# Kernel tuning notes

Measured on AMD Instinct MI355X. Metric: run time of the kernel, lower is better.

## Reference

```python
import jax, jax.numpy as jnp
import numpy as np

N = 50000   # num nodes
E = 800000  # num edges (avg degree 16)
L = 4       # num_blocks
H = 128     # hidden_dim
CD = 3      # coords_dim
VD = 3      # vel_dim
FD = 16     # node feature dim = node_dim - coords_dim - vel_dim
ED = 16     # edge_dim
DIN = 2 * H + ED + 1  # edge MLP input dim = 273


def setup_inputs() -> dict:
    key = jax.random.key(0)
    ks = jax.random.split(key, 32)
    s = 0.05
    inp = {}
    inp['nodes'] = jax.random.normal(ks[0], (N, CD + VD + FD), jnp.float32)
    # avoid self-loops (start==end) so the coord-diff norm is never exactly 0
    start = jax.random.randint(ks[1], (E,), 0, N)
    off = jax.random.randint(ks[2], (E,), 1, N)
    inp['edge_indices'] = jnp.stack([start, (start + off) % N]).astype(jnp.int64)
    inp['edge_features'] = jax.random.normal(ks[3], (E, ED), jnp.float32)
    # node embedding
    inp['emb_w'] = (jax.random.normal(ks[4], (FD, H)) * s).astype(jnp.float32)
    inp['emb_b'] = jnp.zeros((H,), jnp.float32)
    # per-block params, stacked over L blocks
    def w(k, shape):
        return (jax.random.normal(k, shape) * s).astype(jnp.float32)
    inp['ew1'] = w(ks[5], (L, DIN, H)); inp['eb1'] = jnp.zeros((L, H), jnp.float32)
    inp['ew2'] = w(ks[6], (L, H, H));   inp['eb2'] = jnp.zeros((L, H), jnp.float32)
    inp['cw1'] = w(ks[7], (L, H, H));   inp['cb1'] = jnp.zeros((L, H), jnp.float32)
    inp['cw2'] = w(ks[8], (L, H, CD));  inp['cb2'] = jnp.zeros((L, CD), jnp.float32)
    inp['vw1'] = w(ks[9], (L, H, H));   inp['vb1'] = jnp.zeros((L, H), jnp.float32)
    inp['vw2'] = w(ks[10], (L, H, 1));  inp['vb2'] = jnp.zeros((L, 1), jnp.float32)
    inp['nw1'] = w(ks[11], (L, 2 * H, H)); inp['nb1'] = jnp.zeros((L, H), jnp.float32)
    inp['nw2'] = w(ks[12], (L, H, H));  inp['nb2'] = jnp.zeros((L, H), jnp.float32)
    return inp


def _forward(nodes, edge_features, emb_w, emb_b, ew1, eb1, ew2, eb2,
             cw1, cb1, cw2, cb2, vw1, vb1, vw2, vb2, nw1, nb1, nw2, nb2,
             edge_indices):
    silu = jax.nn.silu
    coords = nodes[:, :CD]
    vels = nodes[:, CD:CD + VD]
    h = nodes[:, CD + VD:] @ emb_w + emb_b  # [N, H]
    start, end = edge_indices[0], edge_indices[1]
    n = coords.shape[0]
    # per-node edge counts for the coordinate mean-aggregation
    cnt = jax.ops.segment_sum(jnp.ones((start.shape[0], 1), coords.dtype),
                              start, num_segments=n)
    cnt = jnp.maximum(cnt, 1.0)
    for l in range(L):
        cd = coords[start] - coords[end]                       # [E, CD]
        nrm = jnp.sqrt(jnp.sum(cd * cd, axis=1, keepdims=True))  # [E, 1]
        x = jnp.concatenate([h[start], h[end], nrm, edge_features], axis=1)
        m = silu(silu(x @ ew1[l] + eb1[l]) @ ew2[l] + eb2[l])  # [E, H]
        # coordinate update: mean-aggregated weighted diffs + velocity term
        ct = cd * (silu(m @ cw1[l] + cb1[l]) @ cw2[l] + cb2[l])
        coords = coords + jax.ops.segment_sum(ct, start, num_segments=n) / cnt
        coords = coords + (silu(h @ vw1[l] + vb1[l]) @ vw2[l] + vb2[l]) * vels
        # node update: sum-aggregated messages
        agg = jax.ops.segment_sum(m, start, num_segments=n)    # [N, H]
        h = h + silu(jnp.concatenate([h, agg], axis=1) @ nw1[l] + nb1[l]) @ nw2[l] + nb2[l]
    return coords  # prediction_type == 'coords'


def reference(nodes, edge_indices, edge_features, emb_w, emb_b,
              ew1, eb1, ew2, eb2, cw1, cb1, cw2, cb2,
              vw1, vb1, vw2, vb2, nw1, nb1, nw2, nb2):
    return _forward(nodes, edge_features, emb_w, emb_b, ew1, eb1, ew2, eb2,
                    cw1, cb1, cw2, cb2, vw1, vb1, vw2, vb2,
                    nw1, nb1, nw2, nb2, edge_indices)
```

## Files before the change

### kernel.cpp

```cpp
#include <hip/hip_runtime.h>

constexpr int NN = 50000;
constexpr int EE = 800000;
constexpr int HH = 128;

typedef __attribute__((ext_vector_type(8))) __bf16 bfv8;
typedef __attribute__((ext_vector_type(4))) float f32x4;
typedef unsigned short u16;

__device__ __forceinline__ u16 f2bf(float x){
  unsigned u = __builtin_bit_cast(unsigned, x);
  u = u + 0x7fffu + ((u >> 16) & 1u);
  return (u16)(u >> 16);
}
__device__ __forceinline__ float fsilu(float x){
  return x * __builtin_amdgcn_rcpf(1.f + __expf(-x));
}

__device__ __forceinline__ void stagecpy(u16* __restrict__ dst, const u16* __restrict__ src, int n16){
  const uint4* s = (const uint4*)src;
  uint4* d = (uint4*)dst;
  for (int i = threadIdx.x; i < n16; i += 256) d[i] = s[i];
}

template<int KSTEPS, int CB>
__device__ __forceinline__ void mmW(const u16* Arows, const u16* __restrict__ Bstage,
                                    const float* __restrict__ bias, int NB, f32x4* acc){
  const int lane = threadIdx.x & 63;
  #pragma unroll
  for (int cb = 0; cb < CB; ++cb){
    int col = cb*16 + (lane & 15);
    float b = (col < NB) ? bias[col] : 0.f;
    acc[cb] = (f32x4){b, b, b, b};
  }
  const int arow = lane & 15;
  const char* abase = (const char*)Arows + arow * 256;
  const int kb = (lane >> 4) * 16;
  const int swz = (arow & 7) << 4;
  const bfv8* bq = (const bfv8*)Bstage + lane;
  #pragma unroll
  for (int ks = 0; ks < KSTEPS; ++ks){
    bfv8 a = *(const bfv8*)(abase + ((ks*64 + kb) ^ swz));
    #pragma unroll
    for (int cb = 0; cb < CB; ++cb)
      acc[cb] = __builtin_amdgcn_mfma_f32_16x16x32_bf16(a, bq[(ks*CB + cb) * 64], acc[cb], 0, 0, 0);
  }
}

template<int CB>
__device__ __forceinline__ void silu_store(const f32x4* acc, u16* dst){
  const int lane = threadIdx.x & 63;
  #pragma unroll
  for (int cb = 0; cb < CB; ++cb){
    #pragma unroll
    for (int j = 0; j < 4; ++j){
      int row = ((lane >> 4) << 2) + j;
      int col = cb*16 + (lane & 15);
      *(u16*)((char*)dst + row*256 + ((col*2) ^ ((row & 7) << 4))) = f2bf(fsilu(acc[cb][j]));
    }
  }
}

struct PackDesc { const float* src; u16* dst; int K; int Nc; int CB; int ksteps; int remap; };
struct PackArgs { PackDesc d[32]; };

__global__ __launch_bounds__(256) void pack_kernel(PackArgs pa){
  PackDesc d = pa.d[blockIdx.x];
  int total = d.ksteps * d.CB * 512;
  for (int p = threadIdx.x; p < total; p += 256){
    int j = p & 7, lane = (p >> 3) & 63, cbk = p >> 9;
    int cb = cbk % d.CB, ks = cbk / d.CB;
    int k = ks*32 + ((lane >> 4) * 8) + j;
    int col = cb*16 + (lane & 15);
    int kk = k;
    if (d.remap && k >= 256) kk = (k < 272) ? (k + 1) : ((k == 272) ? 256 : 0x7fffffff);
    float v = (kk < d.K && col < d.Nc) ? d.src[(size_t)kk * d.Nc + col] : 0.f;
    d.dst[p] = f2bf(v);
  }
}

__global__ __launch_bounds__(256) void embed_kernel(const float* __restrict__ nodes,
    const float* __restrict__ emb_w, const float* __restrict__ emb_b,
    float* __restrict__ hf, u16* __restrict__ hbf, float* __restrict__ coords){
  int t = blockIdx.x * 256 + threadIdx.x;
  int g = t >> 2, q = t & 3;
  if (g >= NN) return;
  const float* x = nodes + (size_t)g * 22;
  float acc[32];
  #pragma unroll
  for (int c = 0; c < 32; ++c) acc[c] = emb_b[q*32 + c];
  for (int k = 0; k < 16; ++k){
    float f = x[6 + k];
    const float* wr = emb_w + k*128 + q*32;
    #pragma unroll
    for (int c = 0; c < 32; ++c) acc[c] += f * wr[c];
  }
  size_t off = (size_t)g * HH + q*32;
  #pragma unroll
  for (int c = 0; c < 32; ++c){ hf[off + c] = acc[c]; hbf[off + c] = f2bf(acc[c]); }
  if (q == 0){
    coords[g*3+0] = x[0]; coords[g*3+1] = x[1]; coords[g*3+2] = x[2];
  }
}

__global__ __launch_bounds__(256) void count_kernel(const int* __restrict__ esrc, int* __restrict__ cnt_i){
  int e = blockIdx.x * 256 + threadIdx.x;
  if (e < EE) atomicAdd(&cnt_i[esrc[e]], 1);
}

__global__ __launch_bounds__(256) void scan_kernel(const int* __restrict__ cnt_i,
    int* __restrict__ row_start, int* __restrict__ fill){
  __shared__ int part[256];
  int t = threadIdx.x;
  int lo = t * 196, hi = lo + 196;
  if (lo > NN) lo = NN;
  if (hi > NN) hi = NN;
  int s = 0;
  for (int i = lo; i < hi; ++i) s += cnt_i[i];
  part[t] = s; __syncthreads();
  for (int d = 1; d < 256; d <<= 1){
    int v = (t >= d) ? part[t-d] : 0;
    __syncthreads();
    part[t] += v;
    __syncthreads();
  }
  int run = part[t] - s;
  for (int i = lo; i < hi; ++i){ row_start[i] = run; fill[i] = run; run += cnt_i[i]; }
  if (t == 255) row_start[NN] = run;
}

__global__ __launch_bounds__(256) void scatter_kernel(const int* __restrict__ esrc,
    const int* __restrict__ edst, int* __restrict__ fill,
    int2* __restrict__ sd_sorted, int* __restrict__ eid_sorted){
  int e = blockIdx.x * 256 + threadIdx.x;
  if (e < EE){
    int s = esrc[e];
    int pos = atomicAdd(&fill[s], 1);
    sd_sorted[pos] = make_int2(s, edst[e]);
    eid_sorted[pos] = e;
  }
}

__global__ __launch_bounds__(256) void edge_kernel(
    const float* __restrict__ coords, const u16* __restrict__ hbf, const float* __restrict__ ef,
    const int2* __restrict__ sd_sorted, const int* __restrict__ eid_sorted,
    const u16* __restrict__ ew1p, const u16* __restrict__ ew2p,
    const u16* __restrict__ cw1p, const u16* __restrict__ cw2p,
    const float* __restrict__ eb1, const float* __restrict__ eb2,
    const float* __restrict__ cb1, const float* __restrict__ cb2,
    float* __restrict__ agg, float* __restrict__ acc_ct){
  __shared__ __align__(16) u16 sStage[16384];
  __shared__ __align__(16) u16 sBuf[4][2048];
  __shared__ float4 s_cdn[64];
  __shared__ int s_src[64];
  __shared__ int s_eid[64];

  const int tid = threadIdx.x, wid = tid >> 6, lane = tid & 63;
  const int R = wid * 16;
  const int e0 = blockIdx.x * 64;

  stagecpy(sStage, ew1p, 2048);

  if (lane < 16){
    int row = R + lane;
    int e = e0 + row;
    int2 sd = sd_sorted[e];
    float cx = coords[sd.x*3+0] - coords[sd.y*3+0];
    float cy = coords[sd.x*3+1] - coords[sd.y*3+1];
    float cz = coords[sd.x*3+2] - coords[sd.y*3+2];
    float nrm = sqrtf(cx*cx + cy*cy + cz*cz);
    s_cdn[row] = make_float4(cx, cy, cz, nrm);
    s_src[row] = sd.x; s_eid[row] = eid_sorted[e];
  }

  const int myrow = R + (lane & 15);
  const int g = lane >> 4;
  int2 sd = sd_sorted[e0 + myrow];
  const u16* hsb = hbf + (size_t)sd.x * HH + g*8;
  const u16* hdb = hbf + (size_t)sd.y * HH + g*8;
  u16* sB = sBuf[wid];
  const bfv8* bqs = (const bfv8*)sStage + lane;

  f32x4 acc[8];
  __syncthreads();
  {
    #pragma unroll
    for (int cb = 0; cb < 8; ++cb){
      float b = eb1[cb*16 + (lane & 15)];
      acc[cb] = (f32x4){b, b, b, b};
    }
    #pragma unroll
    for (int ks = 0; ks < 4; ++ks){
      bfv8 a = *(const bfv8*)(hsb + ks*32);
      #pragma unroll
      for (int cb = 0; cb < 8; ++cb)
        acc[cb] = __builtin_amdgcn_mfma_f32_16x16x32_bf16(a, bqs[(ks*8 + cb)*64], acc[cb], 0, 0, 0);
    }
  }
  __syncthreads();
  stagecpy(sStage, ew1p + 4*8*512, 2048);
  __syncthreads();
  {
    #pragma unroll
    for (int ks = 0; ks < 4; ++ks){
      bfv8 a = *(const bfv8*)(hdb + ks*32);
      #pragma unroll
      for (int cb = 0; cb < 8; ++cb)
        acc[cb] = __builtin_amdgcn_mfma_f32_16x16x32_bf16(a, bqs[(ks*8 + cb)*64], acc[cb], 0, 0, 0);
    }
  }
  __syncthreads();
  stagecpy(sStage, ew1p + 8*8*512, 512);
  __syncthreads();
  {
    const int my_eid = s_eid[myrow];
    union { bfv8 v; u16 s[8]; unsigned u[4]; } at;
    at.u[0] = at.u[1] = at.u[2] = at.u[3] = 0u;
    if (g < 2){
      float4 f0 = *(const float4*)(ef + (size_t)my_eid * 16 + g*8);
      float4 f1 = *(const float4*)(ef + (size_t)my_eid * 16 + g*8 + 4);
      at.u[0] = f2bf(f0.x) | ((unsigned)f2bf(f0.y) << 16);
      at.u[1] = f2bf(f0.z) | ((unsigned)f2bf(f0.w) << 16);
      at.u[2] = f2bf(f1.x) | ((unsigned)f2bf(f1.y) << 16);
      at.u[3] = f2bf(f1.z) | ((unsigned)f2bf(f1.w) << 16);
    } else if (g == 2){
      at.s[0] = f2bf(s_cdn[myrow].w);
    }
    #pragma unroll
    for (int cb = 0; cb < 8; ++cb)
      acc[cb] = __builtin_amdgcn_mfma_f32_16x16x32_bf16(at.v, bqs[cb*64], acc[cb], 0, 0, 0);
  }
  silu_store<8>(acc, sB);

  __syncthreads();
  stagecpy(sStage, ew2p, 2048);
  __syncthreads();
  mmW<4, 8>(sB, sStage, eb2, 128, acc);
  {
    const int rb = (lane >> 4) << 2;
    float run[8];
    #pragma unroll
    for (int cb = 0; cb < 8; ++cb) run[cb] = 0.f;
    #pragma unroll
    for (int j = 0; j < 4; ++j){
      int lrow = rb + j, grow = R + lrow;
      int src = s_src[grow];
      bool flush = (j == 3) || (s_src[grow + 1] != src);
      #pragma unroll
      for (int cb = 0; cb < 8; ++cb){
        int col = cb*16 + (lane & 15);
        float m = fsilu(acc[cb][j]);
        run[cb] += m;
        *(u16*)((char*)sB + lrow*256 + ((col*2) ^ ((lrow & 7) << 4))) = f2bf(m);
      }
      if (flush){
        #pragma unroll
        for (int cb = 0; cb < 8; ++cb){
          int col = cb*16 + (lane & 15);
          atomicAdd(&agg[(size_t)src * HH + col], run[cb]);
          run[cb] = 0.f;
        }
      }
    }
  }

  __syncthreads();
  stagecpy(sStage, cw1p, 2048);
  __syncthreads();
  mmW<4, 8>(sB, sStage, cb1, 128, acc);
  silu_store<8>(acc, sB);

  __syncthreads();
  stagecpy(sStage, cw2p, 256);
  __syncthreads();
  f32x4 a4[1];
  mmW<4, 1>(sB, sStage, cb2, 3, a4);
  {
    int col = lane & 15;
    if (col < 3){
      const int rb = (lane >> 4) << 2;
      float run = 0.f;
      #pragma unroll
      for (int j = 0; j < 4; ++j){
        int grow = R + rb + j;
        float4 cdn = s_cdn[grow];
        float cdv = (col == 0) ? cdn.x : ((col == 1) ? cdn.y : cdn.z);
        run += cdv * a4[0][j];
        int src = s_src[grow];
        if (j == 3 || s_src[grow + 1] != src){
          atomicAdd(&acc_ct[(size_t)src * 3 + col], run);
          run = 0.f;
        }
      }
    }
  }
}

__device__ __forceinline__ void mm_lds1(const u16* Arows, const u16* __restrict__ Bp,
                                        const float* __restrict__ bias, int NB, int CBn,
                                        int KS, f32x4* acc){
  const int lane = threadIdx.x & 63;
  for (int cb = 0; cb < CBn; ++cb){
    int col = cb*16 + (lane & 15);
    float b = (col < NB) ? bias[col] : 0.f;
    acc[cb] = (f32x4){b, b, b, b};
  }
  const int arow = lane & 15;
  const char* abase = (const char*)Arows + arow * 256;
  const int kb = (lane >> 4) * 16;
  const int swz = (arow & 7) << 4;
  const bfv8* __restrict__ bq = (const bfv8*)Bp + lane;
  for (int ks = 0; ks < KS; ++ks){
    bfv8 a = *(const bfv8*)(abase + ((ks*64 + kb) ^ swz));
    for (int cb = 0; cb < CBn; ++cb)
      acc[cb] = __builtin_amdgcn_mfma_f32_16x16x32_bf16(a, bq[(ks*CBn + cb) * 64], acc[cb], 0, 0, 0);
  }
}

__global__ __launch_bounds__(256, 4) void node_kernel(
    float* __restrict__ coords, float* __restrict__ hf, u16* __restrict__ hbf,
    const float* __restrict__ agg, const float* __restrict__ acc_ct, const int* __restrict__ row_start,
    const float* __restrict__ nodes,
    const u16* __restrict__ vw1p, const u16* __restrict__ vw2p,
    const u16* __restrict__ nw1p, const u16* __restrict__ nw2p,
    const float* __restrict__ vb1, const float* __restrict__ vb2,
    const float* __restrict__ nb1, const float* __restrict__ nb2){
  __shared__ __align__(16) u16 sV[4][2048];
  __shared__ float s_vt[64];

  const int tid = threadIdx.x, wid = tid >> 6, lane = tid & 63;
  const int R = wid * 16;
  const int g0 = blockIdx.x * 64;

  const int myrow = R + (lane & 15);
  const int gnode = g0 + myrow;
  const int arow = (gnode < NN) ? gnode : (NN - 1);
  const int g = lane >> 4;
  const u16*  hb = hbf + (size_t)arow * HH + g*8;
  const float* ab = agg + (size_t)arow * HH + g*8;

  f32x4 acc[8];
  {
    const bfv8* __restrict__ bq = (const bfv8*)vw1p + lane;
    #pragma unroll
    for (int cb = 0; cb < 8; ++cb){
      float b = vb1[cb*16 + (lane & 15)];
      acc[cb] = (f32x4){b, b, b, b};
    }
    #pragma unroll
    for (int ks = 0; ks < 4; ++ks){
      bfv8 a = *(const bfv8*)(hb + ks*32);
      #pragma unroll
      for (int cb = 0; cb < 8; ++cb)
        acc[cb] = __builtin_amdgcn_mfma_f32_16x16x32_bf16(a, bq[(ks*8 + cb)*64], acc[cb], 0, 0, 0);
    }
  }
  {
    #pragma unroll
    for (int cb = 0; cb < 8; ++cb){
      #pragma unroll
      for (int j = 0; j < 4; ++j){
        int row = ((lane >> 4) << 2) + j;
        int col = cb*16 + (lane & 15);
        *(u16*)((char*)sV[wid] + row*256 + ((col*2) ^ ((row & 7) << 4))) = f2bf(fsilu(acc[cb][j]));
      }
    }
  }
  f32x4 a1[1];
  mm_lds1(sV[wid], vw2p, vb2, 1, 1, 4, a1);
  if ((lane & 15) == 0){
    #pragma unroll
    for (int j = 0; j < 4; ++j) s_vt[R + ((lane >> 4) << 2) + j] = a1[0][j];
  }
  if (lane < 16){
    int row = R + lane, gg = g0 + row;
    if (gg < NN){
      float cn = (float)(row_start[gg + 1] - row_start[gg]);
      if (cn < 1.f) cn = 1.f;
      float vt = s_vt[row];
      #pragma unroll
      for (int c = 0; c < 3; ++c){
        float val = coords[gg*3 + c] + acc_ct[gg*3 + c] / cn + vt * nodes[(size_t)gg*22 + 3 + c];
        coords[gg*3 + c] = val;
      }
    }
  }

  {
    const bfv8* __restrict__ bq = (const bfv8*)nw1p + lane;
    #pragma unroll
    for (int cb = 0; cb < 8; ++cb){
      float b = nb1[cb*16 + (lane & 15)];
      acc[cb] = (f32x4){b, b, b, b};
    }
    #pragma unroll
    for (int ks = 0; ks < 4; ++ks){
      bfv8 a = *(const bfv8*)(hb + ks*32);
      #pragma unroll
      for (int cb = 0; cb < 8; ++cb)
        acc[cb] = __builtin_amdgcn_mfma_f32_16x16x32_bf16(a, bq[(ks*8 + cb)*64], acc[cb], 0, 0, 0);
    }
    #pragma unroll
    for (int ks = 4; ks < 8; ++ks){
      float4 f0 = *(const float4*)(ab + (ks - 4)*32);
      float4 f1 = *(const float4*)(ab + (ks - 4)*32 + 4);
      union { bfv8 v; unsigned u[4]; } aa;
      aa.u[0] = f2bf(f0.x) | ((unsigned)f2bf(f0.y) << 16);
      aa.u[1] = f2bf(f0.z) | ((unsigned)f2bf(f0.w) << 16);
      aa.u[2] = f2bf(f1.x) | ((unsigned)f2bf(f1.y) << 16);
      aa.u[3] = f2bf(f1.z) | ((unsigned)f2bf(f1.w) << 16);
      #pragma unroll
      for (int cb = 0; cb < 8; ++cb)
        acc[cb] = __builtin_amdgcn_mfma_f32_16x16x32_bf16(aa.v, bq[(ks*8 + cb)*64], acc[cb], 0, 0, 0);
    }
  }
  {
    #pragma unroll
    for (int cb = 0; cb < 8; ++cb){
      #pragma unroll
      for (int j = 0; j < 4; ++j){
        int row = ((lane >> 4) << 2) + j;
        int col = cb*16 + (lane & 15);
        *(u16*)((char*)sV[wid] + row*256 + ((col*2) ^ ((row & 7) << 4))) = f2bf(fsilu(acc[cb][j]));
      }
    }
  }
  mm_lds1(sV[wid], nw2p, nb2, 128, 8, 4, acc);
  {
    #pragma unroll
    for (int cb = 0; cb < 8; ++cb){
      int col = cb*16 + (lane & 15);
      #pragma unroll
      for (int j = 0; j < 4; ++j){
        int row = R + ((lane >> 4) << 2) + j, gg = g0 + row;
        if (gg < NN){
          size_t off = (size_t)gg * HH + col;
          float h = acc[cb][j] + hf[off];
          hf[off] = h;
          hbf[off] = f2bf(h);
        }
      }
    }
  }
}

extern "C" void kernel_launch(void* const* d_in, const int* in_sizes, int n_in,
                              void* d_out, int out_size, void* d_ws, size_t ws_size,
                              hipStream_t stream){
  const float* nodes = (const float*)d_in[0];
  const int*   eidx  = (const int*)d_in[1];
  const float* ef    = (const float*)d_in[2];
  const float* emb_w = (const float*)d_in[3];
  const float* emb_b = (const float*)d_in[4];
  const float* ew1 = (const float*)d_in[5];
  const float* eb1 = (const float*)d_in[6];
  const float* ew2 = (const float*)d_in[7];
  const float* eb2 = (const float*)d_in[8];
  const float* cw1 = (const float*)d_in[9];
  const float* cb1 = (const float*)d_in[10];
  const float* cw2 = (const float*)d_in[11];
  const float* cb2 = (const float*)d_in[12];
  const float* vw1 = (const float*)d_in[13];
  const float* vb1 = (const float*)d_in[14];
  const float* vw2 = (const float*)d_in[15];
  const float* vb2 = (const float*)d_in[16];
  const float* nw1 = (const float*)d_in[17];
  const float* nb1 = (const float*)d_in[18];
  const float* nw2 = (const float*)d_in[19];
  const float* nb2 = (const float*)d_in[20];

  constexpr size_t WS_NEEDED = 78u * 1024u * 1024u;
  if (ws_size < WS_NEEDED) return;

  char* ws = (char*)d_ws;
  size_t off = 0;
  auto alloc = [&](size_t bytes){ void* p = ws + off; off += (bytes + 255) & ~(size_t)255; return p; };
  float* coords   = (float*)alloc((size_t)NN * 3 * 4);
  float* hf       = (float*)alloc((size_t)NN * HH * 4);
  u16*   hbf      = (u16*)  alloc((size_t)NN * HH * 2);
  float* agg      = (float*)alloc((size_t)NN * 131 * 4);
  float* acc_ct   = agg + (size_t)NN * HH;
  int*   cnt_i    = (int*)  alloc((size_t)NN * 4);
  int*   row_start= (int*)  alloc((size_t)(NN + 1) * 4);
  int*   fill     = (int*)  alloc((size_t)NN * 4);
  int2*  sd_sorted= (int2*) alloc((size_t)EE * 8);
  int*   eid_sorted=(int*)  alloc((size_t)EE * 4);

  constexpr int O_EW1 = 0;
  constexpr int O_EW2 = O_EW1 + 9*8*512;
  constexpr int O_CW1 = O_EW2 + 4*8*512;
  constexpr int O_CW2 = O_CW1 + 4*8*512;
  constexpr int O_VW1 = O_CW2 + 4*1*512;
  constexpr int O_VW2 = O_VW1 + 4*8*512;
  constexpr int O_NW1 = O_VW2 + 4*1*512;
  constexpr int O_NW2 = O_NW1 + 8*8*512;
  constexpr int LAYER_PACK = O_NW2 + 4*8*512;
  u16* packs = (u16*)alloc((size_t)LAYER_PACK * 4 * 2);

  PackArgs pa;
  for (int l = 0; l < 4; ++l){
    u16* base = packs + (size_t)l * LAYER_PACK;
    int i = l * 8;
    pa.d[i+0] = { ew1 + (size_t)l*273*128, base + O_EW1, 273, 128, 8, 9, 1 };
    pa.d[i+1] = { ew2 + (size_t)l*128*128, base + O_EW2, 128, 128, 8, 4, 0 };
    pa.d[i+2] = { cw1 + (size_t)l*128*128, base + O_CW1, 128, 128, 8, 4, 0 };
    pa.d[i+3] = { cw2 + (size_t)l*128*3,   base + O_CW2, 128,   3, 1, 4, 0 };
    pa.d[i+4] = { vw1 + (size_t)l*128*128, base + O_VW1, 128, 128, 8, 4, 0 };
    pa.d[i+5] = { vw2 + (size_t)l*128*1,   base + O_VW2, 128,   1, 1, 4, 0 };
    pa.d[i+6] = { nw1 + (size_t)l*256*128, base + O_NW1, 256, 128, 8, 8, 0 };
    pa.d[i+7] = { nw2 + (size_t)l*128*128, base + O_NW2, 128, 128, 8, 4, 0 };
  }

  pack_kernel<<<32, 256, 0, stream>>>(pa);
  embed_kernel<<<(NN*4 + 255)/256, 256, 0, stream>>>(nodes, emb_w, emb_b, hf, hbf, coords);
  hipMemsetAsync(cnt_i, 0, (size_t)NN * 4, stream);
  count_kernel<<<(EE + 255)/256, 256, 0, stream>>>(eidx, cnt_i);
  scan_kernel<<<1, 256, 0, stream>>>(cnt_i, row_start, fill);
  scatter_kernel<<<(EE + 255)/256, 256, 0, stream>>>(eidx, eidx + EE, fill, sd_sorted, eid_sorted);

  for (int l = 0; l < 4; ++l){
    hipMemsetAsync(agg, 0, (size_t)NN * 131 * 4, stream);
    u16* base = packs + (size_t)l * LAYER_PACK;
    edge_kernel<<<EE/64, 256, 0, stream>>>(coords, hbf, ef, sd_sorted, eid_sorted,
        base + O_EW1, base + O_EW2, base + O_CW1, base + O_CW2,
        eb1 + l*128, eb2 + l*128, cb1 + l*128, cb2 + l*3, agg, acc_ct);
    node_kernel<<<(NN + 63)/64, 256, 0, stream>>>(coords, hf, hbf, agg, acc_ct, row_start, nodes,
        base + O_VW1, base + O_VW2, base + O_NW1, base + O_NW2,
        vb1 + l*128, vb2 + l, nb1 + l*128, nb2 + l*128);
  }

  hipMemcpyAsync(d_out, coords, (size_t)NN * 3 * 4, hipMemcpyDeviceToDevice, stream);
}
```

Baseline: 2.096 ms.

## Stage all edge weights once in LDS, double block size, drop per-phase barriers

The edge kernel now runs 512 threads over 128 edges per block. It copies the whole first-layer weight matrix and the second-layer matrix into a larger LDS buffer once at kernel start, which removes the repeated stage/barrier cycles between matmul phases. The coordinate MLP weights (cw1, cw2) are read straight from global memory instead of from LDS. The cost is about 104KB of weight staging plus 32KB of buffers in LDS per block, which limits occupancy to one block per CU, and the cw1/cw2 reads now go through global memory or cache.

Result: slower. 2.403 ms (+14.7%).

```diff
diff --git a/kernel.cpp b/kernel.cpp
--- a/kernel.cpp
+++ b/kernel.cpp
@@ -17,14 +17,8 @@
   return x * __builtin_amdgcn_rcpf(1.f + __expf(-x));
 }
 
-__device__ __forceinline__ void stagecpy(u16* __restrict__ dst, const u16* __restrict__ src, int n16){
-  const uint4* s = (const uint4*)src;
-  uint4* d = (uint4*)dst;
-  for (int i = threadIdx.x; i < n16; i += 256) d[i] = s[i];
-}
-
 template<int KSTEPS, int CB>
-__device__ __forceinline__ void mmW(const u16* Arows, const u16* __restrict__ Bstage,
+__device__ __forceinline__ void mmW(const u16* Arows, const u16* Bp,
                                     const float* __restrict__ bias, int NB, f32x4* acc){
   const int lane = threadIdx.x & 63;
   #pragma unroll
@@ -37,7 +31,7 @@
   const char* abase = (const char*)Arows + arow * 256;
   const int kb = (lane >> 4) * 16;
   const int swz = (arow & 7) << 4;
-  const bfv8* bq = (const bfv8*)Bstage + lane;
+  const bfv8* bq = (const bfv8*)Bp + lane;
   #pragma unroll
   for (int ks = 0; ks < KSTEPS; ++ks){
     bfv8 a = *(const bfv8*)(abase + ((ks*64 + kb) ^ swz));
@@ -141,7 +135,7 @@
   }
 }
 
-__global__ __launch_bounds__(256) void edge_kernel(
+__global__ __launch_bounds__(512) void edge_kernel(
     const float* __restrict__ coords, const u16* __restrict__ hbf, const float* __restrict__ ef,
     const int2* __restrict__ sd_sorted, const int* __restrict__ eid_sorted,
     const u16* __restrict__ ew1p, const u16* __restrict__ ew2p,
@@ -149,17 +143,24 @@
     const float* __restrict__ eb1, const float* __restrict__ eb2,
     const float* __restrict__ cb1, const float* __restrict__ cb2,
     float* __restrict__ agg, float* __restrict__ acc_ct){
-  __shared__ __align__(16) u16 sStage[16384];
-  __shared__ __align__(16) u16 sBuf[4][2048];
-  __shared__ float4 s_cdn[64];
-  __shared__ int s_src[64];
-  __shared__ int s_eid[64];
+  __shared__ __align__(16) u16 sStage[53248];
+  __shared__ __align__(16) u16 sBuf[8][2048];
+  __shared__ float4 s_cdn[128];
+  __shared__ int s_src[128];
+  __shared__ int s_eid[128];
 
   const int tid = threadIdx.x, wid = tid >> 6, lane = tid & 63;
   const int R = wid * 16;
-  const int e0 = blockIdx.x * 64;
-
-  stagecpy(sStage, ew1p, 2048);
+  const int e0 = blockIdx.x * 128;
+
+  {
+    const uint4* s1 = (const uint4*)ew1p;
+    uint4* d1 = (uint4*)sStage;
+    for (int i = tid; i < 4608; i += 512) d1[i] = s1[i];
+    const uint4* s2 = (const uint4*)ew2p;
+    uint4* d2 = (uint4*)(sStage + 36864);
+    for (int i = tid; i < 2048; i += 512) d2[i] = s2[i];
+  }
 
   if (lane < 16){
     int row = R + lane;
@@ -172,6 +173,7 @@
     s_cdn[row] = make_float4(cx, cy, cz, nrm);
     s_src[row] = sd.x; s_eid[row] = eid_sorted[e];
   }
+  __syncthreads();
 
   const int myrow = R + (lane & 15);
   const int g = lane >> 4;
@@ -182,7 +184,6 @@
   const bfv8* bqs = (const bfv8*)sStage + lane;
 
   f32x4 acc[8];
-  __syncthreads();
   {
     #pragma unroll
     for (int cb = 0; cb < 8; ++cb){
@@ -196,23 +197,13 @@
       for (int cb = 0; cb < 8; ++cb)
         acc[cb] = __builtin_amdgcn_mfma_f32_16x16x32_bf16(a, bqs[(ks*8 + cb)*64], acc[cb], 0, 0, 0);
     }
-  }
-  __syncthreads();
-  stagecpy(sStage, ew1p + 4*8*512, 2048);
-  __syncthreads();
-  {
-    #pragma unroll
-    for (int ks = 0; ks < 4; ++ks){
-      bfv8 a = *(const bfv8*)(hdb + ks*32);
+    #pragma unroll
+    for (int ks = 4; ks < 8; ++ks){
+      bfv8 a = *(const bfv8*)(hdb + (ks - 4)*32);
       #pragma unroll
       for (int cb = 0; cb < 8; ++cb)
         acc[cb] = __builtin_amdgcn_mfma_f32_16x16x32_bf16(a, bqs[(ks*8 + cb)*64], acc[cb], 0, 0, 0);
     }
-  }
-  __syncthreads();
-  stagecpy(sStage, ew1p + 8*8*512, 512);
-  __syncthreads();
-  {
     const int my_eid = s_eid[myrow];
     union { bfv8 v; u16 s[8]; unsigned u[4]; } at;
     at.u[0] = at.u[1] = at.u[2] = at.u[3] = 0u;
@@ -228,14 +219,11 @@
     }
     #pragma unroll
     for (int cb = 0; cb < 8; ++cb)
-      acc[cb] = __builtin_amdgcn_mfma_f32_16x16x32_bf16(at.v, bqs[cb*64], acc[cb], 0, 0, 0);
+      acc[cb] = __builtin_amdgcn_mfma_f32_16x16x32_bf16(at.v, bqs[(8*8 + cb)*64], acc[cb], 0, 0, 0);
   }
   silu_store<8>(acc, sB);
 
-  __syncthreads();
-  stagecpy(sStage, ew2p, 2048);
-  __syncthreads();
-  mmW<4, 8>(sB, sStage, eb2, 128, acc);
+  mmW<4, 8>(sB, sStage + 36864, eb2, 128, acc);
   {
     const int rb = (lane >> 4) << 2;
     float run[8];
@@ -264,17 +252,11 @@
     }
   }
 
-  __syncthreads();
-  stagecpy(sStage, cw1p, 2048);
-  __syncthreads();
-  mmW<4, 8>(sB, sStage, cb1, 128, acc);
+  mmW<4, 8>(sB, cw1p, cb1, 128, acc);
   silu_store<8>(acc, sB);
 
-  __syncthreads();
-  stagecpy(sStage, cw2p, 256);
-  __syncthreads();
   f32x4 a4[1];
-  mmW<4, 1>(sB, sStage, cb2, 3, a4);
+  mmW<4, 1>(sB, cw2p, cb2, 3, a4);
   {
     int col = lane & 15;
     if (col < 3){
@@ -521,7 +503,7 @@
   for (int l = 0; l < 4; ++l){
     hipMemsetAsync(agg, 0, (size_t)NN * 131 * 4, stream);
     u16* base = packs + (size_t)l * LAYER_PACK;
-    edge_kernel<<<EE/64, 256, 0, stream>>>(coords, hbf, ef, sd_sorted, eid_sorted,
+    edge_kernel<<<EE/128, 512, 0, stream>>>(coords, hbf, ef, sd_sorted, eid_sorted,
         base + O_EW1, base + O_EW2, base + O_CW1, base + O_CW2,
         eb1 + l*128, eb2 + l*128, cb1 + l*128, cb2 + l*3, agg, acc_ct);
     node_kernel<<<(NN + 63)/64, 256, 0, stream>>>(coords, hf, hbf, agg, acc_ct, row_start, nodes,
```
